# Kernel optimization log

Measured on AMD Instinct MI355X. Metric: run time of the kernel, lower is better.

## Reference

```python
import jax, jax.numpy as jnp
import numpy as np
import math

N_HEAD = 16
HEAD_DIM = 64
N_EMBD = N_HEAD * HEAD_DIM  # 1024


def _alibi_slopes(n_heads):
    def pow2(n):
        start = 2.0 ** (-2.0 ** (-(math.log2(n) - 3)))
        return [start * (start ** i) for i in range(n)]
    if n_heads & (n_heads - 1) == 0:
        s = pow2(n_heads)
    else:
        cp2 = 2 ** math.floor(math.log2(n_heads))
        s = pow2(cp2)
        extra_base = 2.0 ** (-2.0 ** (-(math.log2(2 * cp2) - 3)))
        s += [extra_base * (extra_base ** i) for i in range(n_heads - cp2)]
        s = s[:n_heads]
    return jnp.asarray(np.array(s, dtype=np.float32))


def setup_inputs() -> dict:
    key = jax.random.key(0)
    k1, k2, k3, k4 = jax.random.split(key, 4)
    B, T = 2, 2048
    x = jax.random.normal(k1, (B, T, N_EMBD), dtype=jnp.float32)
    # c_attn weight for q,k (use_v=True -> 2*n_embd outputs), no bias
    W_attn = jax.random.normal(k2, (N_EMBD, 2 * N_EMBD), dtype=jnp.float32) * 0.02
    v_tmp = jax.random.normal(k3, (N_HEAD, N_HEAD), dtype=jnp.float32) * 0.02
    proj_tmp = jax.random.normal(k4, (N_HEAD, N_HEAD), dtype=jnp.float32) * 0.02
    return {"x": x, "W_attn": W_attn, "v_tmp": v_tmp, "proj_tmp": proj_tmp}


def reference(x, W_attn, v_tmp, proj_tmp):
    B, T, C = x.shape
    H, D = N_HEAD, HEAD_DIM
    scale = 1.0 / math.sqrt(D)

    qk = x @ W_attn  # (B,T,2C)
    q, k = qk[..., :C], qk[..., C:]
    q = q.reshape(B, T, H, D).transpose(0, 2, 1, 3)  # (B,H,T,D)
    k = k.reshape(B, T, H, D).transpose(0, 2, 1, 3)

    # V via Kronecker-lifted matrix: x @ kron(v_tmp, I_D)
    # block structure => mix head channels: out[...,j,d] = sum_i x[...,i,d]*v_tmp[i,j]
    xh = x.reshape(B, T, H, D)
    v = jnp.einsum('btid,ij->btjd', xh, v_tmp)  # (B,T,H,D)

    scores = jnp.einsum('bhqd,bhkd->bhqk', q, k) * scale  # (B,H,T,T)

    # ALiBi bias + causal mask
    pos = jnp.arange(T, dtype=jnp.float32)
    rel = pos[None, :] - pos[:, None]  # (T,T), mem - ctx
    slopes = _alibi_slopes(H)
    bias = slopes[:, None, None] * rel[None, :, :]
    causal = pos[None, :] <= pos[:, None]
    bias = jnp.where(causal[None, :, :], bias, -jnp.inf)
    scores = scores + bias[None]

    att = jax.nn.softmax(scores, axis=-1)
    y = jnp.einsum('bhqk,bkhd->bqhd', att, v)  # (B,T,H,D)

    # output proj via kron(proj_tmp, I_D).T: out[...,i,d] = sum_j y[...,j,d]*proj_tmp[i,j]
    y = jnp.einsum('btjd,ij->btid', y, proj_tmp)
    return y.reshape(B, T, C)
```

## Files before the change

kernel.cpp:

```cpp
#include <hip/hip_runtime.h>

typedef __attribute__((ext_vector_type(8))) __bf16 bf16x8;
typedef __attribute__((ext_vector_type(8))) unsigned short u16x8;
typedef __attribute__((ext_vector_type(4))) float f32x4;
typedef __attribute__((ext_vector_type(4))) unsigned int u32x4;

#define LOG2E 1.4426950408889634f

#define GLDS16(gp, lp)                                                \
  __builtin_amdgcn_global_load_lds(                                   \
      (const __attribute__((address_space(1))) void*)(gp),            \
      (__attribute__((address_space(3))) void*)(lp), 16, 0, 0)

__device__ __forceinline__ unsigned short f2b(float f) {
  return __builtin_bit_cast(unsigned short, (__bf16)f);
}
__device__ __forceinline__ float b2f(unsigned short h) {
  return __uint_as_float(((unsigned)h) << 16);
}
__device__ __forceinline__ unsigned cvt_pk(float a, float b) {
  unsigned r;
  asm("v_cvt_pk_bf16_f32 %0, %1, %2" : "=v"(r) : "v"(a), "v"(b));
  return r;
}
__device__ __forceinline__ void swap32(unsigned& a, unsigned& b) {
  asm("v_permlane32_swap_b32 %0, %1" : "+v"(a), "+v"(b));
}
__device__ __forceinline__ void swap16(unsigned& a, unsigned& b) {
  asm("v_permlane16_swap_b32 %0, %1" : "+v"(a), "+v"(b));
}
__device__ __forceinline__ float exp2_fast(float x) {
#if __has_builtin(__builtin_amdgcn_exp2f)
  return __builtin_amdgcn_exp2f(x);
#else
  float r; asm("v_exp_f32 %0, %1" : "=v"(r) : "v"(x)); return r;
#endif
}

__global__ __launch_bounds__(256) void k_pre(const float* __restrict__ x,
                                             const float* __restrict__ vt,
                                             const float* __restrict__ W,
                                             unsigned short* __restrict__ xb,
                                             unsigned short* __restrict__ vb,
                                             unsigned short* __restrict__ Wt) {
  if (blockIdx.x < 1024) {
    __shared__ float s_vt[256];
    s_vt[threadIdx.x] = vt[threadIdx.x];
    __syncthreads();
    int g = blockIdx.x * 256 + threadIdx.x;
    int bt = g >> 6, d = g & 63;
    const float* xp = x + (size_t)bt * 1024 + d;
    float xi[16];
#pragma unroll
    for (int i = 0; i < 16; ++i) xi[i] = xp[i * 64];
#pragma unroll
    for (int i = 0; i < 16; ++i) xb[(size_t)bt * 1024 + i * 64 + d] = f2b(xi[i]);
#pragma unroll
    for (int j = 0; j < 16; ++j) {
      float s = 0.f;
#pragma unroll
      for (int i = 0; i < 16; ++i) s += xi[i] * s_vt[i * 16 + j];
      vb[(size_t)bt * 1024 + j * 64 + d] = f2b(s);
    }
  } else {
    __shared__ unsigned short tile[64][65];
    int id2 = blockIdx.x - 1024;
    int n0 = (id2 & 31) * 64;
    int k0 = (id2 >> 5) * 64;
    int tx = threadIdx.x & 63, ty = threadIdx.x >> 6;
#pragma unroll
    for (int r = 0; r < 16; ++r) {
      int kk = ty * 16 + r;
      tile[kk][tx] = f2b(W[(size_t)(k0 + kk) * 2048 + n0 + tx]);
    }
    __syncthreads();
#pragma unroll
    for (int r = 0; r < 16; ++r) {
      int nn = ty * 16 + r;
      Wt[(size_t)(n0 + nn) * 1024 + k0 + tx] = tile[tx][nn];
    }
  }
}

__global__ __launch_bounds__(256) void k_mid(const unsigned short* __restrict__ A,
                                             const unsigned short* __restrict__ Bt,
                                             unsigned short* __restrict__ C,
                                             const unsigned short* __restrict__ vb,
                                             unsigned short* __restrict__ Vt) {
  if (blockIdx.x < 512) {
    __shared__ unsigned short As[128 * 32];
    __shared__ unsigned short Bs[128 * 32];
    const int K = 1024;
    int m0 = (blockIdx.x & 31) * 128;
    int n0 = (blockIdx.x >> 5) * 128;
    int tid = threadIdx.x;
    int w = tid >> 6, lane = tid & 63;
    int lq = lane & 15, lk8 = (lane >> 4) * 8;
    int wr = (w >> 1) * 64, wc = (w & 1) * 64;
    f32x4 acc[4][4];
#pragma unroll
    for (int i = 0; i < 4; ++i)
#pragma unroll
      for (int j = 0; j < 4; ++j)
#pragma unroll
        for (int r = 0; r < 4; ++r) acc[i][j][r] = 0.f;

    for (int kk = 0; kk < K; kk += 32) {
      __syncthreads();
#pragma unroll
      for (int i = 0; i < 2; ++i) {
        int c = tid + 256 * i;
        int row = c >> 2, col = (c & 3) * 8;
        GLDS16(A + (size_t)(m0 + row) * K + kk + col, As + c * 8);
        GLDS16(Bt + (size_t)(n0 + row) * K + kk + col, Bs + c * 8);
      }
      __syncthreads();
      bf16x8 af[4], bf[4];
#pragma unroll
      for (int i = 0; i < 4; ++i) af[i] = *(const bf16x8*)(As + (wr + i * 16 + lq) * 32 + lk8);
#pragma unroll
      for (int j = 0; j < 4; ++j) bf[j] = *(const bf16x8*)(Bs + (wc + j * 16 + lq) * 32 + lk8);
#pragma unroll
      for (int i = 0; i < 4; ++i)
#pragma unroll
        for (int j = 0; j < 4; ++j)
          acc[i][j] = __builtin_amdgcn_mfma_f32_16x16x32_bf16(af[i], bf[j], acc[i][j], 0, 0, 0);
    }
#pragma unroll
    for (int i = 0; i < 4; ++i)
#pragma unroll
      for (int j = 0; j < 4; ++j)
#pragma unroll
        for (int r = 0; r < 4; ++r) {
          int m = m0 + wr + i * 16 + (lane >> 4) * 4 + r;
          int n = n0 + wc + j * 16 + lq;
          C[(size_t)m * 2048 + n] = f2b(acc[i][j][r]);
        }
  } else {
    __shared__ unsigned short tile[64][65];
    int id2 = blockIdx.x - 512;
    int t0 = (id2 & 31) * 64;
    int c0 = ((id2 >> 5) & 15) * 64;
    int b = id2 >> 9;
    int tx = threadIdx.x & 63, ty = threadIdx.x >> 6;
#pragma unroll
    for (int r = 0; r < 16; ++r) {
      int tt = ty * 16 + r;
      tile[tt][tx] = vb[((size_t)b * 2048 + t0 + tt) * 1024 + c0 + tx];
    }
    __syncthreads();
#pragma unroll
    for (int r = 0; r < 16; ++r) {
      int cc = ty * 16 + r;
      Vt[((size_t)b * 1024 + c0 + cc) * 2048 + t0 + tx] = tile[tx][cc];
    }
  }
}

__global__ __launch_bounds__(256, 4) void k_flash(const unsigned short* __restrict__ qkb,
                                                  const unsigned short* __restrict__ Vt,
                                                  unsigned short* __restrict__ y) {
  __shared__ unsigned short Ks[2][2][64 * 32];
  __shared__ unsigned short Vs[2][2][64 * 32];
  int id = blockIdx.x;
  int xcd = id & 7, s = id >> 3;
  int grp = xcd + 8 * (s & 3);
  int v = s >> 2, m = v & 7, t = v >> 3;
  int qt = (t == 0) ? (31 - m) : (t == 1) ? (16 + m) : (t == 2) ? (15 - m) : m;
  int hd = grp & 15, b = grp >> 4;
  int tid = threadIdx.x;
  int w = tid >> 6, lane = tid & 63;
  int quad = lane >> 4, lq = lane & 15, lk8 = quad * 8;
  int xk8 = (quad ^ ((lq >> 1) & 3)) * 8;
  int qh = w >> 1, kh = w & 1;
  int rs = tid >> 2;
  int csw = ((tid & 3) ^ ((tid >> 3) & 3)) * 8;
  const size_t rowb = (size_t)b * 2048;
  const size_t vrow = ((size_t)b * 1024 + hd * 64 + rs) * 2048 + csw;
  const size_t krow = ((rowb + rs) << 11) + 1024 + hd * 64 + csw;

  float slope = exp2f(-0.5f * (float)(hd + 1));
  const float c1 = 0.125f * LOG2E;
  const float c2 = slope * LOG2E;
  const float c16 = 16.0f * c2;
  const float SHIFT = 16.0f;

  bf16x8 ones;
#pragma unroll
  for (int i = 0; i < 8; ++i) ones[i] = (__bf16)1.0f;

  int q0 = qt * 64;
  int qrow = q0 + qh * 32;
  bf16x8 qf[2][2];
#pragma unroll
  for (int qs2 = 0; qs2 < 2; ++qs2) {
    int qg = qrow + qs2 * 16 + lq;
    qf[qs2][0] = *(const bf16x8*)(qkb + ((rowb + qg) << 11) + hd * 64 + lk8);
    qf[qs2][1] = *(const bf16x8*)(qkb + ((rowb + qg) << 11) + hd * 64 + 32 + lk8);
  }
  int kq0 = kh * 32 + quad * 4 - qrow - lq;
  float base0[4];
#pragma unroll
  for (int r = 0; r < 4; ++r) base0[r] = c2 * (float)(kq0 + r) - SHIFT;

  f32x4 o[4][2];
  f32x4 o4[2];
#pragma unroll
  for (int r = 0; r < 4; ++r) { o4[0][r] = 0.f; o4[1][r] = 0.f; }
#pragma unroll
  for (int jj = 0; jj < 4; ++jj)
#pragma unroll
    for (int qs2 = 0; qs2 < 2; ++qs2)
#pragma unroll
      for (int r = 0; r < 4; ++r) o[jj][qs2][r] = 0.f;

  GLDS16(qkb + krow,      &Ks[0][0][rs * 32 + (tid & 3) * 8]);
  GLDS16(qkb + krow + 32, &Ks[0][1][rs * 32 + (tid & 3) * 8]);
  GLDS16(Vt + vrow,       &Vs[0][0][rs * 32 + (tid & 3) * 8]);
  GLDS16(Vt + vrow + 32,  &Vs[0][1][rs * 32 + (tid & 3) * 8]);
  __syncthreads();
  int cur = 0;

#pragma unroll 1
  for (int kt = 0; kt <= qt; ++kt) {
    int k0 = kt * 64;
    if (kt < qt) {
      size_t koff = (size_t)(k0 + 64);
      int nxt = cur ^ 1;
      GLDS16(qkb + krow + (koff << 11),      &Ks[nxt][0][rs * 32 + (tid & 3) * 8]);
      GLDS16(qkb + krow + (koff << 11) + 32, &Ks[nxt][1][rs * 32 + (tid & 3) * 8]);
      GLDS16(Vt + vrow + koff,               &Vs[nxt][0][rs * 32 + (tid & 3) * 8]);
      GLDS16(Vt + vrow + koff + 32,          &Vs[nxt][1][rs * 32 + (tid & 3) * 8]);
    }
    bf16x8 kc[2][2];
#pragma unroll
    for (int ks2 = 0; ks2 < 2; ++ks2) {
      u16x8 t0 = *(const u16x8*)(&Ks[cur][0][(kh * 32 + ks2 * 16 + lq) * 32 + xk8]);
      u16x8 t1 = *(const u16x8*)(&Ks[cur][1][(kh * 32 + ks2 * 16 + lq) * 32 + xk8]);
      kc[ks2][0] = __builtin_bit_cast(bf16x8, t0);
      kc[ks2][1] = __builtin_bit_cast(bf16x8, t1);
    }
    __builtin_amdgcn_s_setprio(1);
    f32x4 S[2][2];
#pragma unroll
    for (int ks2 = 0; ks2 < 2; ++ks2)
#pragma unroll
      for (int qs2 = 0; qs2 < 2; ++qs2) {
        f32x4 a;
#pragma unroll
        for (int r = 0; r < 4; ++r) a[r] = 0.f;
        a = __builtin_amdgcn_mfma_f32_16x16x32_bf16(kc[ks2][0], qf[qs2][0], a, 0, 0, 0);
        a = __builtin_amdgcn_mfma_f32_16x16x32_bf16(kc[ks2][1], qf[qs2][1], a, 0, 0, 0);
        S[ks2][qs2] = a;
      }
    __builtin_amdgcn_s_setprio(0);
    float bk = c2 * (float)k0;
    float p[2][2][4];
    if (kt == qt) {
#pragma unroll
      for (int ks2 = 0; ks2 < 2; ++ks2)
#pragma unroll
        for (int qs2 = 0; qs2 < 2; ++qs2)
#pragma unroll
          for (int r = 0; r < 4; ++r) {
            float vv = S[ks2][qs2][r] * c1 + (base0[r] + bk + c16 * (float)(ks2 - qs2));
            vv = (k0 + kq0 + (ks2 - qs2) * 16 + r <= 0) ? vv : -1e30f;
            p[ks2][qs2][r] = exp2_fast(vv);
          }
    } else {
#pragma unroll
      for (int ks2 = 0; ks2 < 2; ++ks2)
#pragma unroll
        for (int qs2 = 0; qs2 < 2; ++qs2)
#pragma unroll
          for (int r = 0; r < 4; ++r) {
            float vv = S[ks2][qs2][r] * c1 + (base0[r] + bk + c16 * (float)(ks2 - qs2));
            p[ks2][qs2][r] = exp2_fast(vv);
          }
    }
    unsigned pk[2][2][2];
#pragma unroll
    for (int ks2 = 0; ks2 < 2; ++ks2)
#pragma unroll
      for (int qs2 = 0; qs2 < 2; ++qs2) {
        pk[ks2][qs2][0] = cvt_pk(p[ks2][qs2][0], p[ks2][qs2][1]);
        pk[ks2][qs2][1] = cvt_pk(p[ks2][qs2][2], p[ks2][qs2][3]);
      }
    bf16x8 pf[2];
#pragma unroll
    for (int qs2 = 0; qs2 < 2; ++qs2) {
      unsigned a0 = pk[0][qs2][0], b0 = pk[1][qs2][0];
      swap32(a0, b0); swap16(a0, b0);
      unsigned a1 = pk[0][qs2][1], b1 = pk[1][qs2][1];
      swap32(a1, b1); swap16(a1, b1);
      u32x4 tt; tt[0] = a0; tt[1] = a1; tt[2] = b0; tt[3] = b1;
      pf[qs2] = __builtin_bit_cast(bf16x8, tt);
    }
    __builtin_amdgcn_s_setprio(1);
    o4[0] = __builtin_amdgcn_mfma_f32_16x16x32_bf16(ones, pf[0], o4[0], 0, 0, 0);
    o4[1] = __builtin_amdgcn_mfma_f32_16x16x32_bf16(ones, pf[1], o4[1], 0, 0, 0);
#pragma unroll
    for (int jj = 0; jj < 4; ++jj) {
      u16x8 v0 = *(const u16x8*)(&Vs[cur][kh][(jj * 16 + lq) * 32 + xk8]);
      bf16x8 vf = __builtin_bit_cast(bf16x8, v0);
      o[jj][0] = __builtin_amdgcn_mfma_f32_16x16x32_bf16(vf, pf[0], o[jj][0], 0, 0, 0);
      o[jj][1] = __builtin_amdgcn_mfma_f32_16x16x32_bf16(vf, pf[1], o[jj][1], 0, 0, 0);
    }
    __builtin_amdgcn_s_setprio(0);
    if (kt < qt) {
      __syncthreads();
      cur ^= 1;
    }
  }

  __syncthreads();
  float* red0 = (float*)&Ks[0][0][0];
  float* red1 = (float*)&Vs[0][0][0];
  float* red = (qh ? red1 : red0) + lane * 36;
  if (kh == 1) {
#pragma unroll
    for (int jj = 0; jj < 4; ++jj)
#pragma unroll
      for (int qs2 = 0; qs2 < 2; ++qs2)
#pragma unroll
        for (int r = 0; r < 4; ++r) red[(jj * 2 + qs2) * 4 + r] = o[jj][qs2][r];
    red[32] = o4[0][0];
    red[33] = o4[1][0];
  }
  __syncthreads();
  if (kh == 0) {
#pragma unroll
    for (int jj = 0; jj < 4; ++jj)
#pragma unroll
      for (int qs2 = 0; qs2 < 2; ++qs2)
#pragma unroll
        for (int r = 0; r < 4; ++r) o[jj][qs2][r] += red[(jj * 2 + qs2) * 4 + r];
    float inv0 = 1.0f / (o4[0][0] + red[32]);
    float inv1 = 1.0f / (o4[1][0] + red[33]);
#pragma unroll
    for (int qs2 = 0; qs2 < 2; ++qs2) {
      float inv = qs2 ? inv1 : inv0;
      size_t base = ((rowb + qrow + qs2 * 16 + lq) << 10) + hd * 64 + quad * 4;
#pragma unroll
      for (int jj = 0; jj < 4; ++jj) {
        ushort4 pk4;
        pk4.x = f2b(o[jj][qs2][0] * inv);
        pk4.y = f2b(o[jj][qs2][1] * inv);
        pk4.z = f2b(o[jj][qs2][2] * inv);
        pk4.w = f2b(o[jj][qs2][3] * inv);
        *(ushort4*)(y + base + jj * 16) = pk4;
      }
    }
  }
}

__global__ __launch_bounds__(256) void k_proj(const unsigned short* __restrict__ yb,
                                              const float* __restrict__ pt,
                                              float* __restrict__ out) {
  __shared__ float s_pt[256];
  s_pt[threadIdx.x] = pt[threadIdx.x];
  __syncthreads();
  int g = blockIdx.x * 256 + threadIdx.x;
  int bt = g >> 6, d = g & 63;
  float yj[16];
#pragma unroll
  for (int j = 0; j < 16; ++j) yj[j] = b2f(yb[(size_t)bt * 1024 + j * 64 + d]);
#pragma unroll
  for (int i = 0; i < 16; ++i) {
    float s = 0.f;
#pragma unroll
    for (int j = 0; j < 16; ++j) s += yj[j] * s_pt[i * 16 + j];
    out[(size_t)bt * 1024 + i * 64 + d] = s;
  }
}

extern "C" void kernel_launch(void* const* d_in, const int* in_sizes, int n_in,
                              void* d_out, int out_size, void* d_ws, size_t ws_size,
                              hipStream_t stream) {
  const float* x  = (const float*)d_in[0];
  const float* W  = (const float*)d_in[1];
  const float* vt = (const float*)d_in[2];
  const float* pt = (const float*)d_in[3];
  float* out = (float*)d_out;

  char* ws = (char*)d_ws;
  unsigned short* xb  = (unsigned short*)(ws);
  unsigned short* Wt  = (unsigned short*)(ws + (8u  << 20));
  unsigned short* qkb = (unsigned short*)(ws + (12u << 20));
  unsigned short* vb  = (unsigned short*)(ws + (28u << 20));
  unsigned short* Vtr = (unsigned short*)(ws + (36u << 20));
  unsigned short* yb  = xb;

  k_pre  <<<1536, 256, 0, stream>>>(x, vt, W, xb, vb, Wt);
  k_mid  <<<1536, 256, 0, stream>>>(xb, Wt, qkb, vb, Vtr);
  k_flash<<<1024, 256, 0, stream>>>(qkb, Vtr, yb);
  k_proj <<<1024, 256, 0, stream>>>(yb, pt, out);
}
```

Measured before the change: 152.9 us.

## Use 4-stage K/V ring buffer and software-pipeline next tile's QK^T

Replaces the double-buffered K/V shared-memory tiles with a 4-deep ring buffer that prefetches three tiles ahead. Each wait now uses explicit vmcnt counts plus a raw s_barrier instead of a full __syncthreads. The QK^T MFMAs for tile kt+1 are issued inside iteration kt, so they overlap the softmax exponentials and PV MFMAs of the current tile. This is meant to hide global-load latency and keep the matrix units busy, at the cost of doubling LDS per block and adding register pressure for the extra score accumulators.

```diff
diff --git a/kernel.cpp b/kernel.cpp
--- a/kernel.cpp
+++ b/kernel.cpp
@@ -160,8 +160,8 @@
 __global__ __launch_bounds__(256, 4) void k_flash(const unsigned short* __restrict__ qkb,
                                                   const unsigned short* __restrict__ Vt,
                                                   unsigned short* __restrict__ y) {
-  __shared__ unsigned short Ks[2][2][64 * 32];
-  __shared__ unsigned short Vs[2][2][64 * 32];
+  __shared__ unsigned short Ks[4][2][64 * 32];
+  __shared__ unsigned short Vs[4][2][64 * 32];
   int id = blockIdx.x;
   int xcd = id & 7, s = id >> 3;
   int grp = xcd + 8 * (s & 3);
@@ -175,6 +175,7 @@
   int qh = w >> 1, kh = w & 1;
   int rs = tid >> 2;
   int csw = ((tid & 3) ^ ((tid >> 3) & 3)) * 8;
+  int ld = rs * 32 + (tid & 3) * 8;
   const size_t rowb = (size_t)b * 2048;
   const size_t vrow = ((size_t)b * 1024 + hd * 64 + rs) * 2048 + csw;
   const size_t krow = ((rowb + rs) << 11) + 1024 + hd * 64 + csw;
@@ -214,78 +215,122 @@
 #pragma unroll
       for (int r = 0; r < 4; ++r) o[jj][qs2][r] = 0.f;
 
-  GLDS16(qkb + krow,      &Ks[0][0][rs * 32 + (tid & 3) * 8]);
-  GLDS16(qkb + krow + 32, &Ks[0][1][rs * 32 + (tid & 3) * 8]);
-  GLDS16(Vt + vrow,       &Vs[0][0][rs * 32 + (tid & 3) * 8]);
-  GLDS16(Vt + vrow + 32,  &Vs[0][1][rs * 32 + (tid & 3) * 8]);
-  __syncthreads();
-  int cur = 0;
+  GLDS16(qkb + krow,      &Ks[0][0][ld]);
+  GLDS16(qkb + krow + 32, &Ks[0][1][ld]);
+  GLDS16(Vt + vrow,       &Vs[0][0][ld]);
+  GLDS16(Vt + vrow + 32,  &Vs[0][1][ld]);
+  if (qt >= 1) {
+    GLDS16(qkb + krow + ((size_t)64 << 11),      &Ks[1][0][ld]);
+    GLDS16(qkb + krow + ((size_t)64 << 11) + 32, &Ks[1][1][ld]);
+    GLDS16(Vt + vrow + 64,                       &Vs[1][0][ld]);
+    GLDS16(Vt + vrow + 64 + 32,                  &Vs[1][1][ld]);
+  }
+  if (qt >= 2) {
+    GLDS16(qkb + krow + ((size_t)128 << 11),      &Ks[2][0][ld]);
+    GLDS16(qkb + krow + ((size_t)128 << 11) + 32, &Ks[2][1][ld]);
+    GLDS16(Vt + vrow + 128,                       &Vs[2][0][ld]);
+    GLDS16(Vt + vrow + 128 + 32,                  &Vs[2][1][ld]);
+    asm volatile("s_waitcnt vmcnt(4)" ::: "memory");
+  } else {
+    asm volatile("s_waitcnt vmcnt(0)" ::: "memory");
+  }
+  __builtin_amdgcn_s_barrier();
+  __builtin_amdgcn_sched_barrier(0);
+
+  f32x4 Sc[2][2];
+  {
+    bf16x8 kc[2][2];
+#pragma unroll
+    for (int ks2 = 0; ks2 < 2; ++ks2) {
+      u16x8 t0 = *(const u16x8*)(&Ks[0][0][(kh * 32 + ks2 * 16 + lq) * 32 + xk8]);
+      u16x8 t1 = *(const u16x8*)(&Ks[0][1][(kh * 32 + ks2 * 16 + lq) * 32 + xk8]);
+      kc[ks2][0] = __builtin_bit_cast(bf16x8, t0);
+      kc[ks2][1] = __builtin_bit_cast(bf16x8, t1);
+    }
+    __builtin_amdgcn_s_setprio(1);
+#pragma unroll
+    for (int ks2 = 0; ks2 < 2; ++ks2)
+#pragma unroll
+      for (int qs2 = 0; qs2 < 2; ++qs2) {
+        f32x4 a;
+#pragma unroll
+        for (int r = 0; r < 4; ++r) a[r] = 0.f;
+        a = __builtin_amdgcn_mfma_f32_16x16x32_bf16(kc[ks2][0], qf[qs2][0], a, 0, 0, 0);
+        a = __builtin_amdgcn_mfma_f32_16x16x32_bf16(kc[ks2][1], qf[qs2][1], a, 0, 0, 0);
+        Sc[ks2][qs2] = a;
+      }
+    __builtin_amdgcn_s_setprio(0);
+  }
 
 #pragma unroll 1
   for (int kt = 0; kt <= qt; ++kt) {
     int k0 = kt * 64;
+    int cb = kt & 3;
+    if (kt + 3 <= qt) {
+      size_t koff = (size_t)(k0 + 192);
+      int db = (kt + 3) & 3;
+      GLDS16(qkb + krow + (koff << 11),      &Ks[db][0][ld]);
+      GLDS16(qkb + krow + (koff << 11) + 32, &Ks[db][1][ld]);
+      GLDS16(Vt + vrow + koff,               &Vs[db][0][ld]);
+      GLDS16(Vt + vrow + koff + 32,          &Vs[db][1][ld]);
+    }
+    float bk = c2 * (float)k0;
+    unsigned pk[2][2][2];
+    if (kt == qt) {
+#pragma unroll
+      for (int ks2 = 0; ks2 < 2; ++ks2)
+#pragma unroll
+        for (int qs2 = 0; qs2 < 2; ++qs2) {
+          float p[4];
+#pragma unroll
+          for (int r = 0; r < 4; ++r) {
+            float vv = Sc[ks2][qs2][r] * c1 + (base0[r] + bk + c16 * (float)(ks2 - qs2));
+            vv = (k0 + kq0 + (ks2 - qs2) * 16 + r <= 0) ? vv : -1e30f;
+            p[r] = exp2_fast(vv);
+          }
+          pk[ks2][qs2][0] = cvt_pk(p[0], p[1]);
+          pk[ks2][qs2][1] = cvt_pk(p[2], p[3]);
+        }
+    } else {
+#pragma unroll
+      for (int ks2 = 0; ks2 < 2; ++ks2)
+#pragma unroll
+        for (int qs2 = 0; qs2 < 2; ++qs2) {
+          float p[4];
+#pragma unroll
+          for (int r = 0; r < 4; ++r) {
+            float vv = Sc[ks2][qs2][r] * c1 + (base0[r] + bk + c16 * (float)(ks2 - qs2));
+            p[r] = exp2_fast(vv);
+          }
+          pk[ks2][qs2][0] = cvt_pk(p[0], p[1]);
+          pk[ks2][qs2][1] = cvt_pk(p[2], p[3]);
+        }
+    }
+    f32x4 Sn[2][2];
     if (kt < qt) {
-      size_t koff = (size_t)(k0 + 64);
-      int nxt = cur ^ 1;
-      GLDS16(qkb + krow + (koff << 11),      &Ks[nxt][0][rs * 32 + (tid & 3) * 8]);
-      GLDS16(qkb + krow + (koff << 11) + 32, &Ks[nxt][1][rs * 32 + (tid & 3) * 8]);
-      GLDS16(Vt + vrow + koff,               &Vs[nxt][0][rs * 32 + (tid & 3) * 8]);
-      GLDS16(Vt + vrow + koff + 32,          &Vs[nxt][1][rs * 32 + (tid & 3) * 8]);
-    }
-    bf16x8 kc[2][2];
-#pragma unroll
-    for (int ks2 = 0; ks2 < 2; ++ks2) {
-      u16x8 t0 = *(const u16x8*)(&Ks[cur][0][(kh * 32 + ks2 * 16 + lq) * 32 + xk8]);
-      u16x8 t1 = *(const u16x8*)(&Ks[cur][1][(kh * 32 + ks2 * 16 + lq) * 32 + xk8]);
-      kc[ks2][0] = __builtin_bit_cast(bf16x8, t0);
-      kc[ks2][1] = __builtin_bit_cast(bf16x8, t1);
-    }
-    __builtin_amdgcn_s_setprio(1);
-    f32x4 S[2][2];
-#pragma unroll
-    for (int ks2 = 0; ks2 < 2; ++ks2)
-#pragma unroll
-      for (int qs2 = 0; qs2 < 2; ++qs2) {
-        f32x4 a;
-#pragma unroll
-        for (int r = 0; r < 4; ++r) a[r] = 0.f;
-        a = __builtin_amdgcn_mfma_f32_16x16x32_bf16(kc[ks2][0], qf[qs2][0], a, 0, 0, 0);
-        a = __builtin_amdgcn_mfma_f32_16x16x32_bf16(kc[ks2][1], qf[qs2][1], a, 0, 0, 0);
-        S[ks2][qs2] = a;
+      int nb = (kt + 1) & 3;
+      bf16x8 kn[2][2];
+#pragma unroll
+      for (int ks2 = 0; ks2 < 2; ++ks2) {
+        u16x8 t0 = *(const u16x8*)(&Ks[nb][0][(kh * 32 + ks2 * 16 + lq) * 32 + xk8]);
+        u16x8 t1 = *(const u16x8*)(&Ks[nb][1][(kh * 32 + ks2 * 16 + lq) * 32 + xk8]);
+        kn[ks2][0] = __builtin_bit_cast(bf16x8, t0);
+        kn[ks2][1] = __builtin_bit_cast(bf16x8, t1);
       }
-    __builtin_amdgcn_s_setprio(0);
-    float bk = c2 * (float)k0;
-    float p[2][2][4];
-    if (kt == qt) {
+      __builtin_amdgcn_s_setprio(1);
 #pragma unroll
       for (int ks2 = 0; ks2 < 2; ++ks2)
 #pragma unroll
-        for (int qs2 = 0; qs2 < 2; ++qs2)
-#pragma unroll
-          for (int r = 0; r < 4; ++r) {
-            float vv = S[ks2][qs2][r] * c1 + (base0[r] + bk + c16 * (float)(ks2 - qs2));
-            vv = (k0 + kq0 + (ks2 - qs2) * 16 + r <= 0) ? vv : -1e30f;
-            p[ks2][qs2][r] = exp2_fast(vv);
-          }
-    } else {
-#pragma unroll
-      for (int ks2 = 0; ks2 < 2; ++ks2)
-#pragma unroll
-        for (int qs2 = 0; qs2 < 2; ++qs2)
-#pragma unroll
-          for (int r = 0; r < 4; ++r) {
-            float vv = S[ks2][qs2][r] * c1 + (base0[r] + bk + c16 * (float)(ks2 - qs2));
-            p[ks2][qs2][r] = exp2_fast(vv);
-          }
-    }
-    unsigned pk[2][2][2];
-#pragma unroll
-    for (int ks2 = 0; ks2 < 2; ++ks2)
-#pragma unroll
-      for (int qs2 = 0; qs2 < 2; ++qs2) {
-        pk[ks2][qs2][0] = cvt_pk(p[ks2][qs2][0], p[ks2][qs2][1]);
-        pk[ks2][qs2][1] = cvt_pk(p[ks2][qs2][2], p[ks2][qs2][3]);
-      }
+        for (int qs2 = 0; qs2 < 2; ++qs2) {
+          f32x4 a;
+#pragma unroll
+          for (int r = 0; r < 4; ++r) a[r] = 0.f;
+          a = __builtin_amdgcn_mfma_f32_16x16x32_bf16(kn[ks2][0], qf[qs2][0], a, 0, 0, 0);
+          a = __builtin_amdgcn_mfma_f32_16x16x32_bf16(kn[ks2][1], qf[qs2][1], a, 0, 0, 0);
+          Sn[ks2][qs2] = a;
+        }
+      __builtin_amdgcn_s_setprio(0);
+    }
     bf16x8 pf[2];
 #pragma unroll
     for (int qs2 = 0; qs2 < 2; ++qs2) {
@@ -301,15 +346,23 @@
     o4[1] = __builtin_amdgcn_mfma_f32_16x16x32_bf16(ones, pf[1], o4[1], 0, 0, 0);
 #pragma unroll
     for (int jj = 0; jj < 4; ++jj) {
-      u16x8 v0 = *(const u16x8*)(&Vs[cur][kh][(jj * 16 + lq) * 32 + xk8]);
+      u16x8 v0 = *(const u16x8*)(&Vs[cb][kh][(jj * 16 + lq) * 32 + xk8]);
       bf16x8 vf = __builtin_bit_cast(bf16x8, v0);
       o[jj][0] = __builtin_amdgcn_mfma_f32_16x16x32_bf16(vf, pf[0], o[jj][0], 0, 0, 0);
       o[jj][1] = __builtin_amdgcn_mfma_f32_16x16x32_bf16(vf, pf[1], o[jj][1], 0, 0, 0);
     }
     __builtin_amdgcn_s_setprio(0);
     if (kt < qt) {
-      __syncthreads();
-      cur ^= 1;
+      int nf = qt - kt - 1;
+      if (nf >= 2)      asm volatile("s_waitcnt vmcnt(8)" ::: "memory");
+      else if (nf == 1) asm volatile("s_waitcnt vmcnt(4)" ::: "memory");
+      else              asm volatile("s_waitcnt vmcnt(0)" ::: "memory");
+      __builtin_amdgcn_s_barrier();
+      __builtin_amdgcn_sched_barrier(0);
+#pragma unroll
+      for (int ks2 = 0; ks2 < 2; ++ks2)
+#pragma unroll
+        for (int qs2 = 0; qs2 < 2; ++qs2) Sc[ks2][qs2] = Sn[ks2][qs2];
     }
   }
 
```

After: 149.6 us. 2.1% less time.

## Load K and V fragments directly from global memory in flash kernel

Applied to the files above, without the earlier changes.

Drops the double-buffered LDS staging of K and V tiles (global_load_lds plus per-iteration barriers). Each wave now reads its MFMA operands straight from global memory, so the loop no longer needs __syncthreads. The LDS left in use is a small buffer for the final cross-wave reduction. The risk is that waves which used to share a tile through LDS now issue redundant, less coalesced global loads, and there is no prefetch left to hide their latency. The softmax-to-bf16 packing is also interleaved per fragment, and a variable in the GEMM kernel is renamed.

```diff
diff --git a/kernel.cpp b/kernel.cpp
--- a/kernel.cpp
+++ b/kernel.cpp
@@ -132,9 +132,9 @@
       for (int j = 0; j < 4; ++j)
 #pragma unroll
         for (int r = 0; r < 4; ++r) {
-          int m = m0 + wr + i * 16 + (lane >> 4) * 4 + r;
+          int mm = m0 + wr + i * 16 + (lane >> 4) * 4 + r;
           int n = n0 + wc + j * 16 + lq;
-          C[(size_t)m * 2048 + n] = f2b(acc[i][j][r]);
+          C[(size_t)mm * 2048 + n] = f2b(acc[i][j][r]);
         }
   } else {
     __shared__ unsigned short tile[64][65];
@@ -160,8 +160,7 @@
 __global__ __launch_bounds__(256, 4) void k_flash(const unsigned short* __restrict__ qkb,
                                                   const unsigned short* __restrict__ Vt,
                                                   unsigned short* __restrict__ y) {
-  __shared__ unsigned short Ks[2][2][64 * 32];
-  __shared__ unsigned short Vs[2][2][64 * 32];
+  __shared__ float red[2][64 * 36];
   int id = blockIdx.x;
   int xcd = id & 7, s = id >> 3;
   int grp = xcd + 8 * (s & 3);
@@ -171,13 +170,11 @@
   int tid = threadIdx.x;
   int w = tid >> 6, lane = tid & 63;
   int quad = lane >> 4, lq = lane & 15, lk8 = quad * 8;
-  int xk8 = (quad ^ ((lq >> 1) & 3)) * 8;
   int qh = w >> 1, kh = w & 1;
-  int rs = tid >> 2;
-  int csw = ((tid & 3) ^ ((tid >> 3) & 3)) * 8;
   const size_t rowb = (size_t)b * 2048;
-  const size_t vrow = ((size_t)b * 1024 + hd * 64 + rs) * 2048 + csw;
-  const size_t krow = ((rowb + rs) << 11) + 1024 + hd * 64 + csw;
+
+  const unsigned short* kbase = qkb + ((rowb + kh * 32 + lq) << 11) + 1024 + hd * 64 + quad * 8;
+  const unsigned short* vbase = Vt + ((size_t)b * 1024 + hd * 64 + lq) * 2048 + kh * 32 + quad * 8;
 
   float slope = exp2f(-0.5f * (float)(hd + 1));
   const float c1 = 0.125f * LOG2E;
@@ -214,31 +211,15 @@
 #pragma unroll
       for (int r = 0; r < 4; ++r) o[jj][qs2][r] = 0.f;
 
-  GLDS16(qkb + krow,      &Ks[0][0][rs * 32 + (tid & 3) * 8]);
-  GLDS16(qkb + krow + 32, &Ks[0][1][rs * 32 + (tid & 3) * 8]);
-  GLDS16(Vt + vrow,       &Vs[0][0][rs * 32 + (tid & 3) * 8]);
-  GLDS16(Vt + vrow + 32,  &Vs[0][1][rs * 32 + (tid & 3) * 8]);
-  __syncthreads();
-  int cur = 0;
-
 #pragma unroll 1
   for (int kt = 0; kt <= qt; ++kt) {
     int k0 = kt * 64;
-    if (kt < qt) {
-      size_t koff = (size_t)(k0 + 64);
-      int nxt = cur ^ 1;
-      GLDS16(qkb + krow + (koff << 11),      &Ks[nxt][0][rs * 32 + (tid & 3) * 8]);
-      GLDS16(qkb + krow + (koff << 11) + 32, &Ks[nxt][1][rs * 32 + (tid & 3) * 8]);
-      GLDS16(Vt + vrow + koff,               &Vs[nxt][0][rs * 32 + (tid & 3) * 8]);
-      GLDS16(Vt + vrow + koff + 32,          &Vs[nxt][1][rs * 32 + (tid & 3) * 8]);
-    }
     bf16x8 kc[2][2];
 #pragma unroll
     for (int ks2 = 0; ks2 < 2; ++ks2) {
-      u16x8 t0 = *(const u16x8*)(&Ks[cur][0][(kh * 32 + ks2 * 16 + lq) * 32 + xk8]);
-      u16x8 t1 = *(const u16x8*)(&Ks[cur][1][(kh * 32 + ks2 * 16 + lq) * 32 + xk8]);
-      kc[ks2][0] = __builtin_bit_cast(bf16x8, t0);
-      kc[ks2][1] = __builtin_bit_cast(bf16x8, t1);
+      size_t ko = ((size_t)(k0 + ks2 * 16) << 11);
+      kc[ks2][0] = *(const bf16x8*)(kbase + ko);
+      kc[ks2][1] = *(const bf16x8*)(kbase + ko + 32);
     }
     __builtin_amdgcn_s_setprio(1);
     f32x4 S[2][2];
@@ -255,37 +236,37 @@
       }
     __builtin_amdgcn_s_setprio(0);
     float bk = c2 * (float)k0;
-    float p[2][2][4];
+    unsigned pk[2][2][2];
     if (kt == qt) {
 #pragma unroll
       for (int ks2 = 0; ks2 < 2; ++ks2)
 #pragma unroll
-        for (int qs2 = 0; qs2 < 2; ++qs2)
+        for (int qs2 = 0; qs2 < 2; ++qs2) {
+          float p[4];
 #pragma unroll
           for (int r = 0; r < 4; ++r) {
             float vv = S[ks2][qs2][r] * c1 + (base0[r] + bk + c16 * (float)(ks2 - qs2));
             vv = (k0 + kq0 + (ks2 - qs2) * 16 + r <= 0) ? vv : -1e30f;
-            p[ks2][qs2][r] = exp2_fast(vv);
+            p[r] = exp2_fast(vv);
           }
+          pk[ks2][qs2][0] = cvt_pk(p[0], p[1]);
+          pk[ks2][qs2][1] = cvt_pk(p[2], p[3]);
+        }
     } else {
 #pragma unroll
       for (int ks2 = 0; ks2 < 2; ++ks2)
 #pragma unroll
-        for (int qs2 = 0; qs2 < 2; ++qs2)
+        for (int qs2 = 0; qs2 < 2; ++qs2) {
+          float p[4];
 #pragma unroll
           for (int r = 0; r < 4; ++r) {
             float vv = S[ks2][qs2][r] * c1 + (base0[r] + bk + c16 * (float)(ks2 - qs2));
-            p[ks2][qs2][r] = exp2_fast(vv);
+            p[r] = exp2_fast(vv);
           }
-    }
-    unsigned pk[2][2][2];
-#pragma unroll
-    for (int ks2 = 0; ks2 < 2; ++ks2)
-#pragma unroll
-      for (int qs2 = 0; qs2 < 2; ++qs2) {
-        pk[ks2][qs2][0] = cvt_pk(p[ks2][qs2][0], p[ks2][qs2][1]);
-        pk[ks2][qs2][1] = cvt_pk(p[ks2][qs2][2], p[ks2][qs2][3]);
-      }
+          pk[ks2][qs2][0] = cvt_pk(p[0], p[1]);
+          pk[ks2][qs2][1] = cvt_pk(p[2], p[3]);
+        }
+    }
     bf16x8 pf[2];
 #pragma unroll
     for (int qs2 = 0; qs2 < 2; ++qs2) {
@@ -301,31 +282,23 @@
     o4[1] = __builtin_amdgcn_mfma_f32_16x16x32_bf16(ones, pf[1], o4[1], 0, 0, 0);
 #pragma unroll
     for (int jj = 0; jj < 4; ++jj) {
-      u16x8 v0 = *(const u16x8*)(&Vs[cur][kh][(jj * 16 + lq) * 32 + xk8]);
-      bf16x8 vf = __builtin_bit_cast(bf16x8, v0);
+      bf16x8 vf = *(const bf16x8*)(vbase + (size_t)(jj * 16) * 2048 + k0);
       o[jj][0] = __builtin_amdgcn_mfma_f32_16x16x32_bf16(vf, pf[0], o[jj][0], 0, 0, 0);
       o[jj][1] = __builtin_amdgcn_mfma_f32_16x16x32_bf16(vf, pf[1], o[jj][1], 0, 0, 0);
     }
     __builtin_amdgcn_s_setprio(0);
-    if (kt < qt) {
-      __syncthreads();
-      cur ^= 1;
-    }
-  }
-
-  __syncthreads();
-  float* red0 = (float*)&Ks[0][0][0];
-  float* red1 = (float*)&Vs[0][0][0];
-  float* red = (qh ? red1 : red0) + lane * 36;
+  }
+
+  float* rp = &red[qh][lane * 36];
   if (kh == 1) {
 #pragma unroll
     for (int jj = 0; jj < 4; ++jj)
 #pragma unroll
       for (int qs2 = 0; qs2 < 2; ++qs2)
 #pragma unroll
-        for (int r = 0; r < 4; ++r) red[(jj * 2 + qs2) * 4 + r] = o[jj][qs2][r];
-    red[32] = o4[0][0];
-    red[33] = o4[1][0];
+        for (int r = 0; r < 4; ++r) rp[(jj * 2 + qs2) * 4 + r] = o[jj][qs2][r];
+    rp[32] = o4[0][0];
+    rp[33] = o4[1][0];
   }
   __syncthreads();
   if (kh == 0) {
@@ -334,9 +307,9 @@
 #pragma unroll
       for (int qs2 = 0; qs2 < 2; ++qs2)
 #pragma unroll
-        for (int r = 0; r < 4; ++r) o[jj][qs2][r] += red[(jj * 2 + qs2) * 4 + r];
-    float inv0 = 1.0f / (o4[0][0] + red[32]);
-    float inv1 = 1.0f / (o4[1][0] + red[33]);
+        for (int r = 0; r < 4; ++r) o[jj][qs2][r] += rp[(jj * 2 + qs2) * 4 + r];
+    float inv0 = 1.0f / (o4[0][0] + rp[32]);
+    float inv1 = 1.0f / (o4[1][0] + rp[33]);
 #pragma unroll
     for (int qs2 = 0; qs2 < 2; ++qs2) {
       float inv = qs2 ? inv1 : inv0;
```

New measurement: 182.1 us. 19.1% more time.
